# Kernel tuning notes

Measured on AMD Instinct MI355X. Metric: run time of the kernel, lower is better.

## Reference

```python
import jax, jax.numpy as jnp
import numpy as np

N = 8192
CUTOFF_LOWER = 0.0
CUTOFF_UPPER = 5.0
MAX_PAIRS = 64 * N  # max_num_pairs = -64 -> 64 neighbors per atom
BOX_L = 45.0


def setup_inputs() -> dict:
    key = jax.random.key(0)
    k1, _ = jax.random.split(key)
    pos = jax.random.uniform(k1, (N, 3), dtype=jnp.float32) * BOX_L
    batch = jnp.zeros((N,), dtype=jnp.int32)
    return {"pos": pos, "batch": batch}


def reference(pos, batch):
    # Brute O(N^2) neighbor search, cutoff_lower <= r < cutoff_upper,
    # loop=False (no self pairs), include_transpose=True (both (i,j) and (j,i)),
    # resize_to_fit=False: fixed-size output padded with (-1,-1) pairs.
    n = pos.shape[0]
    diff = pos[:, None, :] - pos[None, :, :]          # [N, N, 3] edge_vec = pos_i - pos_j
    d2 = jnp.sum(diff * diff, axis=-1)                 # [N, N]
    same_batch = batch[:, None] == batch[None, :]
    not_self = ~jnp.eye(n, dtype=bool)
    mask = same_batch & not_self & (d2 < CUTOFF_UPPER ** 2) & (d2 >= CUTOFF_LOWER ** 2)
    flat = mask.reshape(-1)
    count = jnp.sum(flat)
    # static-size compaction (jit-compatible): first MAX_PAIRS hits in row-major order
    idx = jnp.nonzero(flat, size=MAX_PAIRS, fill_value=0)[0]
    valid = jnp.arange(MAX_PAIRS) < jnp.minimum(count, MAX_PAIRS)
    i = idx // n
    j = idx % n
    edge_vec = jnp.where(valid[:, None], diff.reshape(n * n, 3)[idx], 0.0)
    d2_g = d2.reshape(-1)[idx]
    edge_weight = jnp.where(valid, jnp.sqrt(jnp.where(valid, d2_g, 1.0)), 0.0)
    edge_index = jnp.stack([jnp.where(valid, i, -1), jnp.where(valid, j, -1)], axis=0)
    edge_index = edge_index.astype(jnp.int64) if jax.config.jax_enable_x64 else edge_index.astype(jnp.int32)
    return edge_index, edge_weight, edge_vec
```

## Files before the change

kernel.cpp:

```cpp
#include <hip/hip_runtime.h>

#define NATOMS 8192
#define MAXP (64 * NATOMS)
#define R2CUT 25.0f

constexpr int NC1 = 9;
constexpr int NCELL = NC1 * NC1 * NC1;
constexpr int BCAP = 48;
constexpr int ROWW = 128;

__device__ __forceinline__ float d2_exact(float dx, float dy, float dz) {
    return __fadd_rn(__fadd_rn(__fmul_rn(dx, dx), __fmul_rn(dy, dy)),
                     __fmul_rn(dz, dz));
}

__device__ __forceinline__ int cellOf(float v) {
    int c = (int)((double)v * 0.2);
    return c < 0 ? 0 : (c > NC1 - 1 ? NC1 - 1 : c);
}

__global__ __launch_bounds__(1024) void bin_all(const float* __restrict__ pos,
                                                int* __restrict__ bucketCount,
                                                float4* __restrict__ buckets) {
    __shared__ unsigned int hist[NCELL];
    const int t = threadIdx.x;
    if (t < NCELL) hist[t] = 0u;
    __syncthreads();
#pragma unroll
    for (int k = 0; k < 8; ++k) {
        const int a = t + k * 1024;
        const float x = pos[3 * a], y = pos[3 * a + 1], z = pos[3 * a + 2];
        const int c = (cellOf(z) * NC1 + cellOf(y)) * NC1 + cellOf(x);
        const int slot = (int)atomicAdd(&hist[c], 1u);
        if (slot < BCAP)
            buckets[c * BCAP + slot] = make_float4(x, y, z, __int_as_float(a));
    }
    __syncthreads();
    if (t < NCELL) bucketCount[t] = (int)hist[t];
}

__global__ __launch_bounds__(512) void nl_neigh(const float* __restrict__ pos,
                                                const int* __restrict__ batch,
                                                const int* __restrict__ bucketCount,
                                                const float4* __restrict__ buckets,
                                                int* __restrict__ counts,
                                                unsigned short* __restrict__ rowbuf) {
    __shared__ unsigned int bm[8][256];
    const int t = threadIdx.x;
    const int lane = t & 63;
    const int wave = t >> 6;
    const int i = blockIdx.x * 8 + wave;
    unsigned int* sb = bm[wave];
    sb[lane] = 0u; sb[lane + 64] = 0u; sb[lane + 128] = 0u; sb[lane + 192] = 0u;

    const float xi = pos[3 * i], yi = pos[3 * i + 1], zi = pos[3 * i + 2];
    const int bi = batch[i];
    const int cx = cellOf(xi), cy = cellOf(yi), cz = cellOf(zi);
    const int xlo = cx > 0 ? cx - 1 : 0;
    const int nc = (cx < NC1 - 1 ? cx + 1 : NC1 - 1) - xlo + 1;

    for (int dz = -1; dz <= 1; ++dz) {
        const int czz = cz + dz;
        if ((unsigned)czz >= (unsigned)NC1) continue;
        for (int dy = -1; dy <= 1; ++dy) {
            const int cyy = cy + dy;
            if ((unsigned)cyy >= (unsigned)NC1) continue;
            const int c0 = (czz * NC1 + cyy) * NC1 + xlo;
            const int n0 = min(bucketCount[c0], BCAP);
            const int n1 = nc > 1 ? min(bucketCount[c0 + 1], BCAP) : 0;
            const int n2 = nc > 2 ? min(bucketCount[c0 + 2], BCAP) : 0;
            const int m = n0 + n1 + n2;
            for (int k = lane; k < m; k += 64) {
                int cell, idx;
                if (k < n0)           { cell = c0;     idx = k; }
                else if (k < n0 + n1) { cell = c0 + 1; idx = k - n0; }
                else                  { cell = c0 + 2; idx = k - n0 - n1; }
                const float4 p = buckets[cell * BCAP + idx];
                const int j = __float_as_int(p.w);
                const float dxv = xi - p.x;
                const float dyv = yi - p.y;
                const float dzv = zi - p.z;
                const float d2 = d2_exact(dxv, dyv, dzv);
                if (d2 < R2CUT && j != i && batch[j] == bi)
                    atomicOr(&sb[j >> 5], 1u << (j & 31));
            }
        }
    }

    unsigned short* rb = rowbuf + (size_t)i * ROWW;
    int total = 0;
#pragma unroll
    for (int g = 0; g < 4; ++g) {
        unsigned int w = sb[g * 64 + lane];
        const int c = __popc(w);
        int incl = c;
        for (int off = 1; off < 64; off <<= 1) {
            const int u = __shfl_up(incl, off);
            if (lane >= off) incl += u;
        }
        int o = total + incl - c;
        const unsigned int jbase = (unsigned)(g * 64 + lane) * 32u;
        while (w) {
            const int bit = __ffs(w) - 1;
            w &= w - 1u;
            if (o < ROWW) rb[o] = (unsigned short)(jbase + (unsigned)bit);
            ++o;
        }
        total += __shfl(incl, 63);
    }
    if (lane == 0) counts[i] = total > ROWW ? ROWW : total;
}

__global__ __launch_bounds__(512) void nl_scatter(const float* __restrict__ pos,
                                                  const unsigned short* __restrict__ rowbuf,
                                                  const int* __restrict__ counts,
                                                  float* __restrict__ out) {
    constexpr int NTHR = 512;
    __shared__ int partial[NTHR];
    __shared__ int rowoff[32];
    const int t = threadIdx.x;
    const int b = blockIdx.x;
    const int lane = t & 63;
    const int wave = t >> 6;

    const int4* c4 = (const int4*)counts;
    int4 v0 = c4[4 * t + 0], v1 = c4[4 * t + 1];
    int4 v2 = c4[4 * t + 2], v3 = c4[4 * t + 3];
    const int s = v0.x + v0.y + v0.z + v0.w + v1.x + v1.y + v1.z + v1.w +
                  v2.x + v2.y + v2.z + v2.w + v3.x + v3.y + v3.z + v3.w;
    partial[t] = s;
    __syncthreads();
    for (int off = 1; off < NTHR; off <<= 1) {
        const int u = (t >= off) ? partial[t - off] : 0;
        __syncthreads();
        partial[t] += u;
        __syncthreads();
    }
    if ((t >> 1) == b) {
        int vals[16];
        vals[0] = v0.x;  vals[1] = v0.y;  vals[2] = v0.z;  vals[3] = v0.w;
        vals[4] = v1.x;  vals[5] = v1.y;  vals[6] = v1.z;  vals[7] = v1.w;
        vals[8] = v2.x;  vals[9] = v2.y;  vals[10] = v2.z; vals[11] = v2.w;
        vals[12] = v3.x; vals[13] = v3.y; vals[14] = v3.z; vals[15] = v3.w;
        const int qb = (t & 1) * 16;
        int run = partial[t] - s;
#pragma unroll
        for (int q = 0; q < 16; ++q) { rowoff[qb + q] = run; run += vals[q]; }
    }
    __syncthreads();
    const int total = partial[NTHR - 1];

    float* __restrict__ outI = out;
    float* __restrict__ outJ = out + MAXP;
    float* __restrict__ outW = out + 2 * MAXP;
    float* __restrict__ outV = out + 3 * MAXP;

    for (int rr = 0; rr < 4; ++rr) {
        const int q = wave * 4 + rr;
        const int i = b * 32 + q;
        const int cnt = counts[i];
        const int base = rowoff[q];
        const float xi = pos[3 * i], yi = pos[3 * i + 1], zi = pos[3 * i + 2];
        const float fi = (float)i;
        const unsigned short* rb = rowbuf + (size_t)i * ROWW;
        for (int k = lane; k < cnt; k += 64) {
            const int j = rb[k];
            const float dxv = xi - pos[3 * j];
            const float dyv = yi - pos[3 * j + 1];
            const float dzv = zi - pos[3 * j + 2];
            const float d2 = d2_exact(dxv, dyv, dzv);
            const int slot = base + k;
            if (slot < MAXP) {
                outI[slot] = fi;
                outJ[slot] = (float)j;
                outW[slot] = sqrtf(d2);
                outV[3 * slot + 0] = dxv;
                outV[3 * slot + 1] = dyv;
                outV[3 * slot + 2] = dzv;
            }
        }
    }

    const int g = b * NTHR + t;
    for (int sl = total + g; sl < MAXP; sl += 256 * NTHR) {
        outI[sl] = -1.f;
        outJ[sl] = -1.f;
        outW[sl] = 0.f;
        outV[3 * sl + 0] = 0.f;
        outV[3 * sl + 1] = 0.f;
        outV[3 * sl + 2] = 0.f;
    }
}

extern "C" void kernel_launch(void* const* d_in, const int* in_sizes, int n_in,
                              void* d_out, int out_size, void* d_ws, size_t ws_size,
                              hipStream_t stream) {
    const float* pos = (const float*)d_in[0];
    const int* batch = (const int*)d_in[1];
    float* out = (float*)d_out;

    char* ws = (char*)d_ws;
    int* counts            = (int*)ws;
    int* bucketCount       = (int*)(ws + (32 << 10));
    float4* buckets        = (float4*)(ws + (64 << 10));
    unsigned short* rowbuf = (unsigned short*)(ws + (640 << 10));

    bin_all<<<1, 1024, 0, stream>>>(pos, bucketCount, buckets);
    nl_neigh<<<NATOMS / 8, 512, 0, stream>>>(pos, batch, bucketCount, buckets,
                                             counts, rowbuf);
    nl_scatter<<<256, 512, 0, stream>>>(pos, rowbuf, counts, out);
}
```

Baseline: 86.23 us.

## Parallelize binning across blocks, prefill padded output there, and hoist cell-count loads

Replaces the single-block binning kernel with a 256-block kernel that uses global atomics on a memset bucket-count array. The same kernel now pre-fills the whole output with -1/0 padding, so the scatter kernel no longer runs a tail-fill loop. The neighbor kernel loads all nine row cell counts up front in an unrolled loop so the loads can overlap. This trades a serial one-block phase for global atomics, an extra memset launch, and a full-output write that the scatter later partly overwrites.

```diff
diff --git a/kernel.cpp b/kernel.cpp
--- a/kernel.cpp
+++ b/kernel.cpp
@@ -19,24 +19,25 @@
     return c < 0 ? 0 : (c > NC1 - 1 ? NC1 - 1 : c);
 }
 
-__global__ __launch_bounds__(1024) void bin_all(const float* __restrict__ pos,
-                                                int* __restrict__ bucketCount,
-                                                float4* __restrict__ buckets) {
-    __shared__ unsigned int hist[NCELL];
-    const int t = threadIdx.x;
-    if (t < NCELL) hist[t] = 0u;
-    __syncthreads();
-#pragma unroll
-    for (int k = 0; k < 8; ++k) {
-        const int a = t + k * 1024;
-        const float x = pos[3 * a], y = pos[3 * a + 1], z = pos[3 * a + 2];
+__global__ __launch_bounds__(256) void bin_par(const float* __restrict__ pos,
+                                               int* __restrict__ bucketCount,
+                                               float4* __restrict__ buckets,
+                                               float4* __restrict__ out4) {
+    const int g = blockIdx.x * 256 + threadIdx.x;
+    const float4 negv  = make_float4(-1.f, -1.f, -1.f, -1.f);
+    const float4 zerov = make_float4(0.f, 0.f, 0.f, 0.f);
+#pragma unroll
+    for (int k = 0; k < 12; ++k) {
+        const int idx = g + k * 65536;
+        out4[idx] = (idx < 262144) ? negv : zerov;
+    }
+    if (g < NATOMS) {
+        const float x = pos[3 * g], y = pos[3 * g + 1], z = pos[3 * g + 2];
         const int c = (cellOf(z) * NC1 + cellOf(y)) * NC1 + cellOf(x);
-        const int slot = (int)atomicAdd(&hist[c], 1u);
+        const int slot = atomicAdd(&bucketCount[c], 1);
         if (slot < BCAP)
-            buckets[c * BCAP + slot] = make_float4(x, y, z, __int_as_float(a));
-    }
-    __syncthreads();
-    if (t < NCELL) bucketCount[t] = (int)hist[t];
+            buckets[c * BCAP + slot] = make_float4(x, y, z, __int_as_float(g));
+    }
 }
 
 __global__ __launch_bounds__(512) void nl_neigh(const float* __restrict__ pos,
@@ -59,31 +60,42 @@
     const int xlo = cx > 0 ? cx - 1 : 0;
     const int nc = (cx < NC1 - 1 ? cx + 1 : NC1 - 1) - xlo + 1;
 
-    for (int dz = -1; dz <= 1; ++dz) {
-        const int czz = cz + dz;
-        if ((unsigned)czz >= (unsigned)NC1) continue;
-        for (int dy = -1; dy <= 1; ++dy) {
-            const int cyy = cy + dy;
-            if ((unsigned)cyy >= (unsigned)NC1) continue;
-            const int c0 = (czz * NC1 + cyy) * NC1 + xlo;
-            const int n0 = min(bucketCount[c0], BCAP);
-            const int n1 = nc > 1 ? min(bucketCount[c0 + 1], BCAP) : 0;
-            const int n2 = nc > 2 ? min(bucketCount[c0 + 2], BCAP) : 0;
-            const int m = n0 + n1 + n2;
-            for (int k = lane; k < m; k += 64) {
-                int cell, idx;
-                if (k < n0)           { cell = c0;     idx = k; }
-                else if (k < n0 + n1) { cell = c0 + 1; idx = k - n0; }
-                else                  { cell = c0 + 2; idx = k - n0 - n1; }
-                const float4 p = buckets[cell * BCAP + idx];
-                const int j = __float_as_int(p.w);
-                const float dxv = xi - p.x;
-                const float dyv = yi - p.y;
-                const float dzv = zi - p.z;
-                const float d2 = d2_exact(dxv, dyv, dzv);
-                if (d2 < R2CUT && j != i && batch[j] == bi)
-                    atomicOr(&sb[j >> 5], 1u << (j & 31));
-            }
+    int c0a[9], n0a[9], n1a[9], n2a[9];
+#pragma unroll
+    for (int r = 0; r < 9; ++r) {
+        const int czz = cz + r / 3 - 1;
+        const int cyy = cy + r % 3 - 1;
+        const bool v = ((unsigned)czz < (unsigned)NC1) &&
+                       ((unsigned)cyy < (unsigned)NC1);
+        c0a[r] = v ? (czz * NC1 + cyy) * NC1 + xlo : 0;
+        n0a[r] = v ? 1 : 0;
+    }
+#pragma unroll
+    for (int r = 0; r < 9; ++r) {
+        const bool v = n0a[r] != 0;
+        n0a[r] = v ? min(bucketCount[c0a[r]], BCAP) : 0;
+        n1a[r] = (v && nc > 1) ? min(bucketCount[c0a[r] + 1], BCAP) : 0;
+        n2a[r] = (v && nc > 2) ? min(bucketCount[c0a[r] + 2], BCAP) : 0;
+    }
+
+#pragma unroll
+    for (int r = 0; r < 9; ++r) {
+        const int n0 = n0a[r], n1 = n1a[r], n2 = n2a[r];
+        const int m = n0 + n1 + n2;
+        const int c0 = c0a[r];
+        for (int k = lane; k < m; k += 64) {
+            int cell, idx;
+            if (k < n0)           { cell = c0;     idx = k; }
+            else if (k < n0 + n1) { cell = c0 + 1; idx = k - n0; }
+            else                  { cell = c0 + 2; idx = k - n0 - n1; }
+            const float4 p = buckets[cell * BCAP + idx];
+            const int j = __float_as_int(p.w);
+            const float dxv = xi - p.x;
+            const float dyv = yi - p.y;
+            const float dzv = zi - p.z;
+            const float d2 = d2_exact(dxv, dyv, dzv);
+            if (d2 < R2CUT && j != i && batch[j] == bi)
+                atomicOr(&sb[j >> 5], 1u << (j & 31));
         }
     }
 
@@ -148,7 +160,6 @@
         for (int q = 0; q < 16; ++q) { rowoff[qb + q] = run; run += vals[q]; }
     }
     __syncthreads();
-    const int total = partial[NTHR - 1];
 
     float* __restrict__ outI = out;
     float* __restrict__ outJ = out + MAXP;
@@ -180,16 +191,6 @@
             }
         }
     }
-
-    const int g = b * NTHR + t;
-    for (int sl = total + g; sl < MAXP; sl += 256 * NTHR) {
-        outI[sl] = -1.f;
-        outJ[sl] = -1.f;
-        outW[sl] = 0.f;
-        outV[3 * sl + 0] = 0.f;
-        outV[3 * sl + 1] = 0.f;
-        outV[3 * sl + 2] = 0.f;
-    }
 }
 
 extern "C" void kernel_launch(void* const* d_in, const int* in_sizes, int n_in,
@@ -205,7 +206,8 @@
     float4* buckets        = (float4*)(ws + (64 << 10));
     unsigned short* rowbuf = (unsigned short*)(ws + (640 << 10));
 
-    bin_all<<<1, 1024, 0, stream>>>(pos, bucketCount, buckets);
+    hipMemsetAsync(bucketCount, 0, NCELL * sizeof(int), stream);
+    bin_par<<<256, 256, 0, stream>>>(pos, bucketCount, buckets, (float4*)out);
     nl_neigh<<<NATOMS / 8, 512, 0, stream>>>(pos, batch, bucketCount, buckets,
                                              counts, rowbuf);
     nl_scatter<<<256, 512, 0, stream>>>(pos, rowbuf, counts, out);
```

After: 88.80 us. 3.0% more time.

## Batch all 9 neighbor-row loads up front and store batch ids alongside buckets

Applied to the files above, without the earlier changes.

The neighbor search now computes all nine cell-row descriptors first, then issues every bucket and batch load for the first 64 candidates before any distance tests run, exposing memory-level parallelism instead of serialising load-then-compute per row. Batch ids are copied into a parallel bucketBatch array during binning, so the inner loop no longer does a dependent gather batch[j]. This raises register pressure (9 float4 plus 9 ints per lane) and adds one extra store per atom in the single-block binning kernel.

```diff
diff --git a/kernel.cpp b/kernel.cpp
--- a/kernel.cpp
+++ b/kernel.cpp
@@ -20,8 +20,10 @@
 }
 
 __global__ __launch_bounds__(1024) void bin_all(const float* __restrict__ pos,
+                                                const int* __restrict__ batch,
                                                 int* __restrict__ bucketCount,
-                                                float4* __restrict__ buckets) {
+                                                float4* __restrict__ buckets,
+                                                int* __restrict__ bucketBatch) {
     __shared__ unsigned int hist[NCELL];
     const int t = threadIdx.x;
     if (t < NCELL) hist[t] = 0u;
@@ -32,8 +34,10 @@
         const float x = pos[3 * a], y = pos[3 * a + 1], z = pos[3 * a + 2];
         const int c = (cellOf(z) * NC1 + cellOf(y)) * NC1 + cellOf(x);
         const int slot = (int)atomicAdd(&hist[c], 1u);
-        if (slot < BCAP)
+        if (slot < BCAP) {
             buckets[c * BCAP + slot] = make_float4(x, y, z, __int_as_float(a));
+            bucketBatch[c * BCAP + slot] = batch[a];
+        }
     }
     __syncthreads();
     if (t < NCELL) bucketCount[t] = (int)hist[t];
@@ -43,6 +47,7 @@
                                                 const int* __restrict__ batch,
                                                 const int* __restrict__ bucketCount,
                                                 const float4* __restrict__ buckets,
+                                                const int* __restrict__ bucketBatch,
                                                 int* __restrict__ counts,
                                                 unsigned short* __restrict__ rowbuf) {
     __shared__ unsigned int bm[8][256];
@@ -59,29 +64,69 @@
     const int xlo = cx > 0 ? cx - 1 : 0;
     const int nc = (cx < NC1 - 1 ? cx + 1 : NC1 - 1) - xlo + 1;
 
-    for (int dz = -1; dz <= 1; ++dz) {
-        const int czz = cz + dz;
-        if ((unsigned)czz >= (unsigned)NC1) continue;
-        for (int dy = -1; dy <= 1; ++dy) {
-            const int cyy = cy + dy;
-            if ((unsigned)cyy >= (unsigned)NC1) continue;
-            const int c0 = (czz * NC1 + cyy) * NC1 + xlo;
-            const int n0 = min(bucketCount[c0], BCAP);
-            const int n1 = nc > 1 ? min(bucketCount[c0 + 1], BCAP) : 0;
-            const int n2 = nc > 2 ? min(bucketCount[c0 + 2], BCAP) : 0;
-            const int m = n0 + n1 + n2;
-            for (int k = lane; k < m; k += 64) {
-                int cell, idx;
-                if (k < n0)           { cell = c0;     idx = k; }
-                else if (k < n0 + n1) { cell = c0 + 1; idx = k - n0; }
-                else                  { cell = c0 + 2; idx = k - n0 - n1; }
-                const float4 p = buckets[cell * BCAP + idx];
+    int c0a[9], n0a[9], n1a[9], n2a[9];
+#pragma unroll
+    for (int r = 0; r < 9; ++r) {
+        const int czz = cz + r / 3 - 1;
+        const int cyy = cy + r % 3 - 1;
+        const bool v = ((unsigned)czz < (unsigned)NC1) &&
+                       ((unsigned)cyy < (unsigned)NC1);
+        c0a[r] = v ? (czz * NC1 + cyy) * NC1 + xlo : 0;
+        n0a[r] = v ? 1 : 0;
+    }
+#pragma unroll
+    for (int r = 0; r < 9; ++r) {
+        const bool v = n0a[r] != 0;
+        n0a[r] = v ? min(bucketCount[c0a[r]], BCAP) : 0;
+        n1a[r] = (v && nc > 1) ? min(bucketCount[c0a[r] + 1], BCAP) : 0;
+        n2a[r] = (v && nc > 2) ? min(bucketCount[c0a[r] + 2], BCAP) : 0;
+    }
+
+    float4 pr[9];
+    int    br[9];
+    int    ma[9];
+#pragma unroll
+    for (int r = 0; r < 9; ++r) {
+        const int n0 = n0a[r], n01 = n0 + n1a[r];
+        const int m = n01 + n2a[r];
+        ma[r] = m;
+        int cell = c0a[r], idx = lane;
+        if (lane >= n0)  { cell = c0a[r] + 1; idx = lane - n0; }
+        if (lane >= n01) { cell = c0a[r] + 2; idx = lane - n01; }
+        if (lane >= m)   { cell = c0a[r];     idx = 0; }
+        const int off = cell * BCAP + idx;
+        pr[r] = buckets[off];
+        br[r] = bucketBatch[off];
+    }
+#pragma unroll
+    for (int r = 0; r < 9; ++r) {
+        if (lane < ma[r]) {
+            const float4 p = pr[r];
+            const int j = __float_as_int(p.w);
+            const float dxv = xi - p.x;
+            const float dyv = yi - p.y;
+            const float dzv = zi - p.z;
+            const float d2 = d2_exact(dxv, dyv, dzv);
+            if (d2 < R2CUT && j != i && br[r] == bi)
+                atomicOr(&sb[j >> 5], 1u << (j & 31));
+        }
+    }
+#pragma unroll
+    for (int r = 0; r < 9; ++r) {
+        if (__builtin_expect(ma[r] > 64, 0)) {
+            const int n0 = n0a[r], n01 = n0 + n1a[r];
+            for (int k = 64 + lane; k < ma[r]; k += 64) {
+                int cell = c0a[r], idx = k;
+                if (k >= n0)  { cell = c0a[r] + 1; idx = k - n0; }
+                if (k >= n01) { cell = c0a[r] + 2; idx = k - n01; }
+                const int off = cell * BCAP + idx;
+                const float4 p = buckets[off];
                 const int j = __float_as_int(p.w);
                 const float dxv = xi - p.x;
                 const float dyv = yi - p.y;
                 const float dzv = zi - p.z;
                 const float d2 = d2_exact(dxv, dyv, dzv);
-                if (d2 < R2CUT && j != i && batch[j] == bi)
+                if (d2 < R2CUT && j != i && bucketBatch[off] == bi)
                     atomicOr(&sb[j >> 5], 1u << (j & 31));
             }
         }
@@ -203,10 +248,12 @@
     int* counts            = (int*)ws;
     int* bucketCount       = (int*)(ws + (32 << 10));
     float4* buckets        = (float4*)(ws + (64 << 10));
-    unsigned short* rowbuf = (unsigned short*)(ws + (640 << 10));
-
-    bin_all<<<1, 1024, 0, stream>>>(pos, bucketCount, buckets);
+    int* bucketBatch       = (int*)(ws + (640 << 10));
+    unsigned short* rowbuf = (unsigned short*)(ws + (800 << 10));
+
+    bin_all<<<1, 1024, 0, stream>>>(pos, batch, bucketCount, buckets,
+                                    bucketBatch);
     nl_neigh<<<NATOMS / 8, 512, 0, stream>>>(pos, batch, bucketCount, buckets,
-                                             counts, rowbuf);
+                                             bucketBatch, counts, rowbuf);
     nl_scatter<<<256, 512, 0, stream>>>(pos, rowbuf, counts, out);
 }
```

Result: slower. 98.31 us (+14.0%).

## Fuse cell binning into neighbor kernel with per-block shared-memory counting sort

Applied to the files above, without the earlier changes.

Removes the single-block global binning kernel. Each of 256 blocks now redundantly counting-sorts all atoms into cells held in about 158 KB of dynamic shared memory (SoA positions, batch, ids, cell starts), then processes 32 rows by reading candidates from LDS. This drops one launch and its serial dependency, along with global bucket reads and the bucket capacity limit. In exchange, every block repeats the full sort, and occupancy is one block per CU.

```diff
diff --git a/kernel.cpp b/kernel.cpp
--- a/kernel.cpp
+++ b/kernel.cpp
@@ -6,8 +6,10 @@
 
 constexpr int NC1 = 9;
 constexpr int NCELL = NC1 * NC1 * NC1;
-constexpr int BCAP = 48;
 constexpr int ROWW = 128;
+constexpr int APT = NATOMS / 512;
+
+constexpr int SMEM_BYTES = 161536;
 
 __device__ __forceinline__ float d2_exact(float dx, float dy, float dz) {
     return __fadd_rn(__fadd_rn(__fmul_rn(dx, dx), __fmul_rn(dy, dy)),
@@ -19,96 +21,127 @@
     return c < 0 ? 0 : (c > NC1 - 1 ? NC1 - 1 : c);
 }
 
-__global__ __launch_bounds__(1024) void bin_all(const float* __restrict__ pos,
-                                                int* __restrict__ bucketCount,
-                                                float4* __restrict__ buckets) {
-    __shared__ unsigned int hist[NCELL];
-    const int t = threadIdx.x;
-    if (t < NCELL) hist[t] = 0u;
-    __syncthreads();
-#pragma unroll
-    for (int k = 0; k < 8; ++k) {
-        const int a = t + k * 1024;
-        const float x = pos[3 * a], y = pos[3 * a + 1], z = pos[3 * a + 2];
-        const int c = (cellOf(z) * NC1 + cellOf(y)) * NC1 + cellOf(x);
-        const int slot = (int)atomicAdd(&hist[c], 1u);
-        if (slot < BCAP)
-            buckets[c * BCAP + slot] = make_float4(x, y, z, __int_as_float(a));
-    }
-    __syncthreads();
-    if (t < NCELL) bucketCount[t] = (int)hist[t];
-}
-
-__global__ __launch_bounds__(512) void nl_neigh(const float* __restrict__ pos,
-                                                const int* __restrict__ batch,
-                                                const int* __restrict__ bucketCount,
-                                                const float4* __restrict__ buckets,
-                                                int* __restrict__ counts,
-                                                unsigned short* __restrict__ rowbuf) {
-    __shared__ unsigned int bm[8][256];
+__global__ void __launch_bounds__(512) nl_main(const float* __restrict__ pos,
+                                               const int* __restrict__ batch,
+                                               int* __restrict__ counts,
+                                               unsigned short* __restrict__ rowbuf) {
+    extern __shared__ char smem[];
+    float* xs = (float*)smem;
+    float* ys = xs + NATOMS;
+    float* zs = ys + NATOMS;
+    int* bt = (int*)(zs + NATOMS);
+    unsigned short* id = (unsigned short*)(bt + NATOMS);
+    int* cellStart = (int*)(smem + 147456);
+    int* cursor    = (int*)(smem + 150400);
+    unsigned int* bmAll = (unsigned int*)(smem + 153344);
+
     const int t = threadIdx.x;
     const int lane = t & 63;
     const int wave = t >> 6;
-    const int i = blockIdx.x * 8 + wave;
-    unsigned int* sb = bm[wave];
-    sb[lane] = 0u; sb[lane + 64] = 0u; sb[lane + 128] = 0u; sb[lane + 192] = 0u;
-
-    const float xi = pos[3 * i], yi = pos[3 * i + 1], zi = pos[3 * i + 2];
-    const int bi = batch[i];
-    const int cx = cellOf(xi), cy = cellOf(yi), cz = cellOf(zi);
-    const int xlo = cx > 0 ? cx - 1 : 0;
-    const int nc = (cx < NC1 - 1 ? cx + 1 : NC1 - 1) - xlo + 1;
-
-    for (int dz = -1; dz <= 1; ++dz) {
-        const int czz = cz + dz;
-        if ((unsigned)czz >= (unsigned)NC1) continue;
-        for (int dy = -1; dy <= 1; ++dy) {
-            const int cyy = cy + dy;
-            if ((unsigned)cyy >= (unsigned)NC1) continue;
-            const int c0 = (czz * NC1 + cyy) * NC1 + xlo;
-            const int n0 = min(bucketCount[c0], BCAP);
-            const int n1 = nc > 1 ? min(bucketCount[c0 + 1], BCAP) : 0;
-            const int n2 = nc > 2 ? min(bucketCount[c0 + 2], BCAP) : 0;
-            const int m = n0 + n1 + n2;
-            for (int k = lane; k < m; k += 64) {
-                int cell, idx;
-                if (k < n0)           { cell = c0;     idx = k; }
-                else if (k < n0 + n1) { cell = c0 + 1; idx = k - n0; }
-                else                  { cell = c0 + 2; idx = k - n0 - n1; }
-                const float4 p = buckets[cell * BCAP + idx];
-                const int j = __float_as_int(p.w);
-                const float dxv = xi - p.x;
-                const float dyv = yi - p.y;
-                const float dzv = zi - p.z;
-                const float d2 = d2_exact(dxv, dyv, dzv);
-                if (d2 < R2CUT && j != i && batch[j] == bi)
-                    atomicOr(&sb[j >> 5], 1u << (j & 31));
-            }
-        }
-    }
-
-    unsigned short* rb = rowbuf + (size_t)i * ROWW;
-    int total = 0;
-#pragma unroll
-    for (int g = 0; g < 4; ++g) {
-        unsigned int w = sb[g * 64 + lane];
-        const int c = __popc(w);
-        int incl = c;
+    const int b = blockIdx.x;
+
+    for (int c = t; c < 736; c += 512) cursor[c] = 0;
+    __syncthreads();
+    int pc[APT];
+#pragma unroll
+    for (int k = 0; k < APT; ++k) {
+        const int a = t + k * 512;
+        const float x = pos[3 * a], y = pos[3 * a + 1], z = pos[3 * a + 2];
+        pc[k] = (cellOf(z) * NC1 + cellOf(y)) * NC1 + cellOf(x);
+        atomicAdd((unsigned int*)&cursor[pc[k]], 1u);
+    }
+    __syncthreads();
+    if (wave == 0) {
+        int loc[12];
+        int sum = 0;
+#pragma unroll
+        for (int k = 0; k < 12; ++k) {
+            const int c = lane * 12 + k;
+            loc[k] = (c < NCELL) ? cursor[c] : 0;
+            sum += loc[k];
+        }
+        int incl = sum;
         for (int off = 1; off < 64; off <<= 1) {
             const int u = __shfl_up(incl, off);
             if (lane >= off) incl += u;
         }
-        int o = total + incl - c;
-        const unsigned int jbase = (unsigned)(g * 64 + lane) * 32u;
-        while (w) {
-            const int bit = __ffs(w) - 1;
-            w &= w - 1u;
-            if (o < ROWW) rb[o] = (unsigned short)(jbase + (unsigned)bit);
-            ++o;
-        }
-        total += __shfl(incl, 63);
-    }
-    if (lane == 0) counts[i] = total > ROWW ? ROWW : total;
+        int run = incl - sum;
+#pragma unroll
+        for (int k = 0; k < 12; ++k) {
+            const int c = lane * 12 + k;
+            if (c < NCELL) cellStart[c] = run;
+            run += loc[k];
+        }
+        if (lane == 63)
+            for (int c = NCELL; c < 736; ++c) cellStart[c] = NATOMS;
+    }
+    __syncthreads();
+    for (int c = t; c < 736; c += 512) cursor[c] = cellStart[c];
+    __syncthreads();
+#pragma unroll
+    for (int k = 0; k < APT; ++k) {
+        const int a = t + k * 512;
+        const int s = atomicAdd((unsigned int*)&cursor[pc[k]], 1u);
+        xs[s] = pos[3 * a];
+        ys[s] = pos[3 * a + 1];
+        zs[s] = pos[3 * a + 2];
+        bt[s] = batch[a];
+        id[s] = (unsigned short)a;
+    }
+    __syncthreads();
+
+    unsigned int* sb = bmAll + wave * 256;
+    for (int rr = 0; rr < 4; ++rr) {
+        const int q = wave * 4 + rr;
+        const int i = b * 32 + q;
+        sb[lane] = 0u; sb[lane + 64] = 0u; sb[lane + 128] = 0u; sb[lane + 192] = 0u;
+        const float xi = pos[3 * i], yi = pos[3 * i + 1], zi = pos[3 * i + 2];
+        const int bi = batch[i];
+        const int cx = cellOf(xi), cy = cellOf(yi), cz = cellOf(zi);
+        const int xlo = cx > 0 ? cx - 1 : 0;
+        const int nc = (cx < NC1 - 1 ? cx + 1 : NC1 - 1) - xlo + 1;
+#pragma unroll
+        for (int r = 0; r < 9; ++r) {
+            const int czz = cz + r / 3 - 1;
+            const int cyy = cy + r % 3 - 1;
+            if ((unsigned)czz >= (unsigned)NC1 || (unsigned)cyy >= (unsigned)NC1)
+                continue;
+            const int c0 = (czz * NC1 + cyy) * NC1 + xlo;
+            const int s0 = cellStart[c0];
+            const int e0 = cellStart[c0 + nc];
+            for (int k = s0 + lane; k < e0; k += 64) {
+                const float dxv = xi - xs[k];
+                const float dyv = yi - ys[k];
+                const float dzv = zi - zs[k];
+                const float d2 = d2_exact(dxv, dyv, dzv);
+                const int j = id[k];
+                if (d2 < R2CUT && j != i && bt[k] == bi)
+                    atomicOr(&sb[j >> 5], 1u << (j & 31));
+            }
+        }
+        unsigned short* rb = rowbuf + (size_t)i * ROWW;
+        int total = 0;
+#pragma unroll
+        for (int g = 0; g < 4; ++g) {
+            unsigned int w = sb[g * 64 + lane];
+            const int c = __popc(w);
+            int incl = c;
+            for (int off = 1; off < 64; off <<= 1) {
+                const int u = __shfl_up(incl, off);
+                if (lane >= off) incl += u;
+            }
+            int o = total + incl - c;
+            const unsigned int jbase = (unsigned)(g * 64 + lane) * 32u;
+            while (w) {
+                const int bit = __ffs(w) - 1;
+                w &= w - 1u;
+                if (o < ROWW) rb[o] = (unsigned short)(jbase + (unsigned)bit);
+                ++o;
+            }
+            total += __shfl(incl, 63);
+        }
+        if (lane == 0) counts[i] = total > ROWW ? ROWW : total;
+    }
 }
 
 __global__ __launch_bounds__(512) void nl_scatter(const float* __restrict__ pos,
@@ -201,12 +234,10 @@
 
     char* ws = (char*)d_ws;
     int* counts            = (int*)ws;
-    int* bucketCount       = (int*)(ws + (32 << 10));
-    float4* buckets        = (float4*)(ws + (64 << 10));
-    unsigned short* rowbuf = (unsigned short*)(ws + (640 << 10));
-
-    bin_all<<<1, 1024, 0, stream>>>(pos, bucketCount, buckets);
-    nl_neigh<<<NATOMS / 8, 512, 0, stream>>>(pos, batch, bucketCount, buckets,
-                                             counts, rowbuf);
+    unsigned short* rowbuf = (unsigned short*)(ws + (32 << 10));
+
+    hipFuncSetAttribute((const void*)nl_main,
+                        hipFuncAttributeMaxDynamicSharedMemorySize, SMEM_BYTES);
+    nl_main<<<256, 512, SMEM_BYTES, stream>>>(pos, batch, counts, rowbuf);
     nl_scatter<<<256, 512, 0, stream>>>(pos, rowbuf, counts, out);
 }
```

Result: slower. 90.68 us (+5.2%).
